# Optimization experiments

Hardware: AMD Instinct MI355X
Metric: run time of the kernel (lower is better)

The kernel has to match this reference:

```python
import jax, jax.numpy as jnp
import numpy as np

V, D, J = 1024, 1024, 1024  # num_outputs, predictor_dim, joiner_dim
B, U = 64, 512
NULL_INDEX = 0


def setup_inputs() -> dict:
    key = jax.random.key(0)
    ks = jax.random.split(key, 9)
    s = 0.02
    return {
        "y": jax.random.randint(ks[0], (B, U), 0, V, dtype=jnp.int64) if jax.config.jax_enable_x64 else jax.random.randint(ks[0], (B, U), 0, V, dtype=jnp.int32),
        "embed": jax.random.normal(ks[1], (V, D), jnp.float32) * s,
        "weight_ih": jax.random.normal(ks[2], (3 * D, D), jnp.float32) * s,
        "bias_ih": jax.random.normal(ks[3], (3 * D,), jnp.float32) * s,
        "weight_hh": jax.random.normal(ks[4], (3 * D, D), jnp.float32) * s,
        "bias_hh": jax.random.normal(ks[5], (3 * D,), jnp.float32) * s,
        "linear_w": jax.random.normal(ks[6], (J, D), jnp.float32) * s,
        "linear_b": jax.random.normal(ks[7], (J,), jnp.float32) * s,
        "initial_state": jax.random.normal(ks[8], (D,), jnp.float32),
    }


def reference(y, embed, weight_ih, bias_ih, weight_hh, bias_hh, linear_w, linear_b, initial_state):
    b, u_len = y.shape
    d = initial_state.shape[0]
    # Decoder input sequence: start symbol (NULL_INDEX=0) then the labels -> length U+1
    tokens = jnp.concatenate([jnp.full((b, 1), NULL_INDEX, dtype=y.dtype), y], axis=1)  # [B, U+1]
    x = embed[tokens]  # [B, U+1, D]
    # Precompute input-side gate pre-activations for all steps (batched GEMM)
    gx = jnp.einsum("bud,gd->bug", x, weight_ih) + bias_ih  # [B, U+1, 3D]
    h0 = jnp.broadcast_to(initial_state, (b, d))

    def step(h, gx_t):
        # PyTorch GRUCell: gates ordered (r, z, n)
        gh = h @ weight_hh.T + bias_hh  # [B, 3D]
        r = jax.nn.sigmoid(gx_t[:, :d] + gh[:, :d])
        z = jax.nn.sigmoid(gx_t[:, d:2 * d] + gh[:, d:2 * d])
        n = jnp.tanh(gx_t[:, 2 * d:] + r * gh[:, 2 * d:])
        h_new = (1.0 - z) * n + z * h
        return h_new, h_new

    _, hs = jax.lax.scan(step, h0, jnp.swapaxes(gx, 0, 1))  # hs: [U+1, B, D]
    out = jnp.einsum("ubd,jd->buj", hs, linear_w) + linear_b  # [B, U+1, J]
    return out
```

## Files before the change

### kernel.cpp

```cpp
#include <hip/hip_runtime.h>
#include <hip/hip_bf16.h>

typedef float f32x4 __attribute__((ext_vector_type(4)));
typedef short s16x8 __attribute__((ext_vector_type(8)));
typedef int   i32x4 __attribute__((ext_vector_type(4)));
typedef _Float16 h16x8 __attribute__((ext_vector_type(8)));

#define NV 1024
#define ND 1024
#define NJ 1024
#define NB 64
#define NU 512
#define NT 513
#define G3 3072
#define SLOT 65536
#define NWG 64
#define CANARY 0x7FFF7FFFu

static __device__ __forceinline__ unsigned short f2h(float f) {
  union { _Float16 h; unsigned short u; } x; x.h = (_Float16)f;
  return x.u;
}

static __device__ __forceinline__ void unswizzle(long e, int& r, int& k) {
  long blk = e >> 9; int l = (int)((e >> 3) & 63); int j = (int)(e & 7);
  r = (int)(blk >> 5) * 16 + (l & 15);
  k = ((int)(blk & 31)) * 32 + ((l >> 4) << 3) + j;
}

__global__ void predictor_prep(const float* __restrict__ whh, const float* __restrict__ wih,
                               const float* __restrict__ em, const float* __restrict__ lw,
                               const float* __restrict__ bih, const float* __restrict__ bhh,
                               const float* __restrict__ init,
                               unsigned short* __restrict__ wh_sw, unsigned short* __restrict__ wi_sw,
                               unsigned short* __restrict__ em_sw, unsigned short* __restrict__ lw_sw,
                               float* __restrict__ bias_sum, unsigned short* __restrict__ hs) {
  long e = (long)blockIdx.x * 256 + threadIdx.x;
  const long nbig = 3145728, nsm = 1048576;
  if (e < nbig) { int r, k; unswizzle(e, r, k); wh_sw[e] = f2h(whh[(long)r * 1024 + k]); return; }
  e -= nbig;
  if (e < nbig) { int r, k; unswizzle(e, r, k); wi_sw[e] = f2h(wih[(long)r * 1024 + k]); return; }
  e -= nbig;
  if (e < nsm) { int r, k; unswizzle(e, r, k); em_sw[e] = f2h(em[(long)r * 1024 + k]); return; }
  e -= nsm;
  if (e < nsm) { int r, k; unswizzle(e, r, k); lw_sw[e] = f2h(lw[(long)r * 1024 + k]); return; }
  e -= nsm;
  if (e < 65536) { int r, k; unswizzle(e, r, k); hs[e] = f2h(init[k]); return; }
  e -= 65536;
  if (e < 3072) { bias_sum[e] = bih[e] + bhh[e]; return; }
  e -= 3072;
  if (e < 4202496) {
    s16x8 c = { (short)0x7FFF, (short)0x7FFF, (short)0x7FFF, (short)0x7FFF,
                (short)0x7FFF, (short)0x7FFF, (short)0x7FFF, (short)0x7FFF };
    *(s16x8*)(hs + 65536 + e * 8) = c;
  }
}

__global__ __launch_bounds__(256) void predictor_gemm(
    const unsigned short* __restrict__ A, long a_chunk_stride,
    const unsigned short* __restrict__ Bw,
    const float* __restrict__ bias, float* __restrict__ out,
    int rowmul_i, int rowmul_c, int out_stride) {
  const int nt = blockIdx.x, chunk = blockIdx.y;
  const int tid = threadIdx.x, lane = tid & 63, wave = tid >> 6;
  const unsigned short* Ab = A + (long)chunk * a_chunk_stride + wave * 16384 + lane * 8;
  const unsigned short* Bb = Bw + (long)nt * 65536 + lane * 8;
  f32x4 a0 = {0,0,0,0}, a1 = {0,0,0,0}, a2 = {0,0,0,0}, a3 = {0,0,0,0};
#pragma unroll 4
  for (int kc = 0; kc < 32; ++kc) {
    h16x8 av = __builtin_bit_cast(h16x8, *(const s16x8*)(Ab + kc * 512));
    h16x8 w0 = __builtin_bit_cast(h16x8, *(const s16x8*)(Bb + kc * 512));
    h16x8 w1 = __builtin_bit_cast(h16x8, *(const s16x8*)(Bb + 16384 + kc * 512));
    h16x8 w2 = __builtin_bit_cast(h16x8, *(const s16x8*)(Bb + 32768 + kc * 512));
    h16x8 w3 = __builtin_bit_cast(h16x8, *(const s16x8*)(Bb + 49152 + kc * 512));
    a0 = __builtin_amdgcn_mfma_f32_16x16x32_f16(av, w0, a0, 0, 0, 0);
    a1 = __builtin_amdgcn_mfma_f32_16x16x32_f16(av, w1, a1, 0, 0, 0);
    a2 = __builtin_amdgcn_mfma_f32_16x16x32_f16(av, w2, a2, 0, 0, 0);
    a3 = __builtin_amdgcn_mfma_f32_16x16x32_f16(av, w3, a3, 0, 0, 0);
  }
  const int q = lane >> 4, nl = lane & 15, colbase = nt << 6;
#pragma unroll
  for (int j = 0; j < 4; ++j) {
    int il = (wave << 4) + (q << 2) + j;
    long row = (long)il * rowmul_i + (long)chunk * rowmul_c;
    float* orow = out + row * out_stride + colbase;
    orow[nl]      = a0[j] + bias[colbase + nl];
    orow[16 + nl] = a1[j] + bias[colbase + 16 + nl];
    orow[32 + nl] = a2[j] + bias[colbase + 32 + nl];
    orow[48 + nl] = a3[j] + bias[colbase + 48 + nl];
  }
}

#define PINSTAGE(CNT, B)                                                        \
  asm volatile("s_waitcnt vmcnt(" #CNT ")"                                      \
    : "+v"(hf[(B)*8+0]), "+v"(hf[(B)*8+1]), "+v"(hf[(B)*8+2]), "+v"(hf[(B)*8+3]), \
      "+v"(hf[(B)*8+4]), "+v"(hf[(B)*8+5]), "+v"(hf[(B)*8+6]), "+v"(hf[(B)*8+7]) :: "memory")

#define PVALID(B, CNT)                                                          \
  {                                                                             \
    PINSTAGE(CNT, B);                                                           \
    for (;;) {                                                                  \
      int ok = 1;                                                               \
      _Pragma("unroll")                                                         \
      for (int i = 0; i < 8; ++i) {                                             \
        i32x4 v = hf[(B)*8 + i];                                                \
        ok &= (v[0] != (int)CANARY) & (v[1] != (int)CANARY) &                   \
              (v[2] != (int)CANARY) & (v[3] != (int)CANARY);                    \
      }                                                                         \
      if (__all(ok)) break;                                                     \
      __builtin_amdgcn_s_sleep(1);                                              \
      _Pragma("unroll")                                                         \
      for (int i = 0; i < 8; ++i) {                                             \
        const unsigned short* a2_ = hprev + (B)*16384 + ((w<<3)+i)*512 + lane*8;\
        asm volatile("global_load_dwordx4 %0, %1, off sc1"                      \
                     : "=v"(hf[(B)*8+i]) : "v"(a2_) : "memory");                \
      }                                                                         \
      PINSTAGE(0, B);                                                           \
    }                                                                           \
  }

__global__ __launch_bounds__(256, 1) void predictor_rnn(
    const unsigned short* __restrict__ wh_sw, const float* __restrict__ gtab,
    const int* __restrict__ y, const float* __restrict__ init,
    unsigned short* __restrict__ hs) {
  __shared__ float buf[4][3][4][64][4];
  __shared__ unsigned short tbuf[1024];
  const int wg = blockIdx.x, tid = threadIdx.x, lane = tid & 63, w = tid >> 6;
  const int q = lane >> 4, dloc = lane & 15, dg = (wg << 4) + dloc;

  h16x8 wrf[8], wzf[8], wnf[8];
#pragma unroll
  for (int i = 0; i < 8; ++i) {
    int kc = (w << 3) + i;
    wrf[i] = __builtin_bit_cast(h16x8, *(const s16x8*)(wh_sw + ((long)(      wg) << 14) + kc * 512 + lane * 8));
    wzf[i] = __builtin_bit_cast(h16x8, *(const s16x8*)(wh_sw + ((long)( 64 + wg) << 14) + kc * 512 + lane * 8));
    wnf[i] = __builtin_bit_cast(h16x8, *(const s16x8*)(wh_sw + ((long)(128 + wg) << 14) + kc * 512 + lane * 8));
  }
  float hreg[4];
#pragma unroll
  for (int j = 0; j < 4; ++j) hreg[j] = init[dg];

  for (int t = 1; t <= NT; ++t) {
    float gr[4], gz[4], gn[4];
#pragma unroll
    for (int j = 0; j < 4; ++j) {
      int b = (w << 4) + (q << 2) + j;
      int tok = (t == 1) ? 0 : y[b * NU + (t - 2)];
      const float* g = gtab + (long)tok * G3 + dg;
      asm volatile("global_load_dword %0, %1, off" : "=v"(gr[j]) : "v"(g) : "memory");
      asm volatile("global_load_dword %0, %1, off" : "=v"(gz[j]) : "v"(g + 1024) : "memory");
      asm volatile("global_load_dword %0, %1, off" : "=v"(gn[j]) : "v"(g + 2048) : "memory");
    }

    const unsigned short* hprev = hs + (long)(t - 1) * SLOT;
    unsigned short* hcur = hs + (long)t * SLOT;

    i32x4 hf[32];
#pragma unroll
    for (int bg = 0; bg < 4; ++bg)
#pragma unroll
      for (int i = 0; i < 8; ++i) {
        const unsigned short* a = hprev + bg * 16384 + ((w << 3) + i) * 512 + lane * 8;
        asm volatile("global_load_dwordx4 %0, %1, off sc1" : "=v"(hf[bg * 8 + i]) : "v"(a) : "memory");
      }
    f32x4 aR[4], aZ[4], aN[4];
#pragma unroll
    for (int bg = 0; bg < 4; ++bg) { aR[bg] = (f32x4){0,0,0,0}; aZ[bg] = (f32x4){0,0,0,0}; aN[bg] = (f32x4){0,0,0,0}; }

    PVALID(0, 24);
#pragma unroll
    for (int i = 0; i < 8; ++i) { h16x8 a = __builtin_bit_cast(h16x8, hf[0 * 8 + i]);
      aR[0] = __builtin_amdgcn_mfma_f32_16x16x32_f16(a, wrf[i], aR[0], 0, 0, 0);
      aZ[0] = __builtin_amdgcn_mfma_f32_16x16x32_f16(a, wzf[i], aZ[0], 0, 0, 0);
      aN[0] = __builtin_amdgcn_mfma_f32_16x16x32_f16(a, wnf[i], aN[0], 0, 0, 0); }
    PVALID(1, 16);
#pragma unroll
    for (int i = 0; i < 8; ++i) { h16x8 a = __builtin_bit_cast(h16x8, hf[1 * 8 + i]);
      aR[1] = __builtin_amdgcn_mfma_f32_16x16x32_f16(a, wrf[i], aR[1], 0, 0, 0);
      aZ[1] = __builtin_amdgcn_mfma_f32_16x16x32_f16(a, wzf[i], aZ[1], 0, 0, 0);
      aN[1] = __builtin_amdgcn_mfma_f32_16x16x32_f16(a, wnf[i], aN[1], 0, 0, 0); }
    PVALID(2, 8);
#pragma unroll
    for (int i = 0; i < 8; ++i) { h16x8 a = __builtin_bit_cast(h16x8, hf[2 * 8 + i]);
      aR[2] = __builtin_amdgcn_mfma_f32_16x16x32_f16(a, wrf[i], aR[2], 0, 0, 0);
      aZ[2] = __builtin_amdgcn_mfma_f32_16x16x32_f16(a, wzf[i], aZ[2], 0, 0, 0);
      aN[2] = __builtin_amdgcn_mfma_f32_16x16x32_f16(a, wnf[i], aN[2], 0, 0, 0); }
    PVALID(3, 0);
#pragma unroll
    for (int i = 0; i < 8; ++i) { h16x8 a = __builtin_bit_cast(h16x8, hf[3 * 8 + i]);
      aR[3] = __builtin_amdgcn_mfma_f32_16x16x32_f16(a, wrf[i], aR[3], 0, 0, 0);
      aZ[3] = __builtin_amdgcn_mfma_f32_16x16x32_f16(a, wzf[i], aZ[3], 0, 0, 0);
      aN[3] = __builtin_amdgcn_mfma_f32_16x16x32_f16(a, wnf[i], aN[3], 0, 0, 0); }

    asm volatile("s_waitcnt vmcnt(0)"
      : "+v"(gr[0]), "+v"(gr[1]), "+v"(gr[2]), "+v"(gr[3]),
        "+v"(gz[0]), "+v"(gz[1]), "+v"(gz[2]), "+v"(gz[3]),
        "+v"(gn[0]), "+v"(gn[1]), "+v"(gn[2]), "+v"(gn[3]) :: "memory");

#pragma unroll
    for (int b2 = 0; b2 < 4; ++b2)
      if (b2 != w) {
        *(f32x4*)&buf[w][0][b2][lane][0] = aR[b2];
        *(f32x4*)&buf[w][1][b2][lane][0] = aZ[b2];
        *(f32x4*)&buf[w][2][b2][lane][0] = aN[b2];
      }
    __syncthreads();
    f32x4 sR = aR[w], sZ = aZ[w], sN = aN[w];
#pragma unroll
    for (int v = 0; v < 4; ++v)
      if (v != w) {
        sR += *(const f32x4*)&buf[v][0][w][lane][0];
        sZ += *(const f32x4*)&buf[v][1][w][lane][0];
        sN += *(const f32x4*)&buf[v][2][w][lane][0];
      }
    __syncthreads();

#pragma unroll
    for (int j = 0; j < 4; ++j) {
      float r = 1.f / (1.f + __expf(-(gr[j] + sR[j])));
      float z = 1.f / (1.f + __expf(-(gz[j] + sZ[j])));
      float np = gn[j] + r * sN[j];
      float e2 = __expf(-2.f * fabsf(np));
      float tn = (1.f - e2) / (1.f + e2);
      tn = np < 0.f ? -tn : tn;
      float hnew = (1.f - z) * tn + z * hreg[j];
      hreg[j] = hnew;
      tbuf[(w << 8) + ((((q << 2) + j) | ((dloc >> 3) << 4)) << 3) + (dloc & 7)] = f2h(hnew);
    }
    asm volatile("s_waitcnt lgkmcnt(0)" ::: "memory");

    {
      unsigned long long pv = *(const unsigned long long*)(tbuf + (w << 8) + lane * 4);
      unsigned short* gp = hcur + ((long)(w * 32 + (wg >> 1)) << 9) + ((wg & 1) << 8) + lane * 4;
      asm volatile("global_store_dwordx2 %0, %1, off sc1" :: "v"(gp), "v"(pv) : "memory");
    }
  }
}

extern "C" void kernel_launch(void* const* d_in, const int* in_sizes, int n_in,
                              void* d_out, int out_size, void* d_ws, size_t ws_size,
                              hipStream_t stream) {
  const int*   y    = (const int*)d_in[0];
  const float* em   = (const float*)d_in[1];
  const float* wih  = (const float*)d_in[2];
  const float* bih  = (const float*)d_in[3];
  const float* whh  = (const float*)d_in[4];
  const float* bhh  = (const float*)d_in[5];
  const float* lw   = (const float*)d_in[6];
  const float* lb   = (const float*)d_in[7];
  const float* init = (const float*)d_in[8];
  float* out = (float*)d_out;

  char* ws = (char*)d_ws;
  size_t off = 0;
  auto alloc = [&](size_t n) { void* p = ws + off; off += (n + 255) & ~(size_t)255; return p; };
  unsigned short* wh_sw   = (unsigned short*)alloc(6291456);
  unsigned short* wi_sw   = (unsigned short*)alloc(6291456);
  unsigned short* em_sw   = (unsigned short*)alloc(2097152);
  unsigned short* lw_sw   = (unsigned short*)alloc(2097152);
  float*          gtab    = (float*)alloc(12582912);
  float*          bias_sum= (float*)alloc(12288);
  unsigned short* hs      = (unsigned short*)alloc(67371008UL);
  (void)ws_size; (void)in_sizes; (void)n_in; (void)out_size;

  predictor_prep<<<dim3(49452), dim3(256), 0, stream>>>(
      whh, wih, em, lw, bih, bhh, init, wh_sw, wi_sw, em_sw, lw_sw, bias_sum, hs);
  predictor_gemm<<<dim3(48, 16), dim3(256), 0, stream>>>(
      em_sw, 65536L, wi_sw, bias_sum, gtab, 1, 64, 3072);
  predictor_rnn<<<dim3(NWG), dim3(256), 0, stream>>>(wh_sw, gtab, y, init, hs);
  predictor_gemm<<<dim3(16, 513), dim3(256), 0, stream>>>(
      hs + 65536, 65536L, lw_sw, lb, out, 513, 1, 1024);
}
```

Before: 3.425 ms.

## Fuse output projection into RNN kernel with per-step flag-driven consumer workgroups

Merges the recurrent GRU kernel and the final output-projection GEMM into one persistent launch. 64 workgroups run the recurrence and publish a per-wave step counter in padded flag slots, and 192 extra workgroups poll those flags and compute output tiles for finished timesteps while later steps are still running. The RNN workgroups now also wait on the flags of all producer waves before loading the previous hidden state, in addition to the existing canary check. This hides the output GEMM behind the serial recurrence, at the cost of polling traffic, more memory contention on the RNN critical path, and a dependence on all 256 workgroups being co-resident.

```diff
diff --git a/kernel.cpp b/kernel.cpp
--- a/kernel.cpp
+++ b/kernel.cpp
@@ -15,6 +15,9 @@
 #define G3 3072
 #define SLOT 65536
 #define NWG 64
+#define NOUT 192
+#define NTILE 8208
+#define FSTRIDE 32
 #define CANARY 0x7FFF7FFFu
 
 static __device__ __forceinline__ unsigned short f2h(float f) {
@@ -34,7 +37,8 @@
                                const float* __restrict__ init,
                                unsigned short* __restrict__ wh_sw, unsigned short* __restrict__ wi_sw,
                                unsigned short* __restrict__ em_sw, unsigned short* __restrict__ lw_sw,
-                               float* __restrict__ bias_sum, unsigned short* __restrict__ hs) {
+                               float* __restrict__ bias_sum, unsigned short* __restrict__ hs,
+                               unsigned int* __restrict__ flags) {
   long e = (long)blockIdx.x * 256 + threadIdx.x;
   const long nbig = 3145728, nsm = 1048576;
   if (e < nbig) { int r, k; unswizzle(e, r, k); wh_sw[e] = f2h(whh[(long)r * 1024 + k]); return; }
@@ -49,7 +53,9 @@
   e -= 65536;
   if (e < 3072) { bias_sum[e] = bih[e] + bhh[e]; return; }
   e -= 3072;
-  if (e < 4202496) {
+  if (e < 8192) { flags[e] = 0u; return; }
+  e -= 8192;
+  if (e < 4202752) {
     s16x8 c = { (short)0x7FFF, (short)0x7FFF, (short)0x7FFF, (short)0x7FFF,
                 (short)0x7FFF, (short)0x7FFF, (short)0x7FFF, (short)0x7FFF };
     *(s16x8*)(hs + 65536 + e * 8) = c;
@@ -119,120 +125,205 @@
     }                                                                           \
   }
 
-__global__ __launch_bounds__(256, 1) void predictor_rnn(
+__global__ __launch_bounds__(256, 1) void predictor_fused(
     const unsigned short* __restrict__ wh_sw, const float* __restrict__ gtab,
     const int* __restrict__ y, const float* __restrict__ init,
-    unsigned short* __restrict__ hs) {
+    unsigned short* __restrict__ hs, unsigned int* __restrict__ flags,
+    const unsigned short* __restrict__ lw_sw, const float* __restrict__ lb,
+    float* __restrict__ out) {
   __shared__ float buf[4][3][4][64][4];
   __shared__ unsigned short tbuf[1024];
   const int wg = blockIdx.x, tid = threadIdx.x, lane = tid & 63, w = tid >> 6;
-  const int q = lane >> 4, dloc = lane & 15, dg = (wg << 4) + dloc;
-
-  h16x8 wrf[8], wzf[8], wnf[8];
-#pragma unroll
-  for (int i = 0; i < 8; ++i) {
-    int kc = (w << 3) + i;
-    wrf[i] = __builtin_bit_cast(h16x8, *(const s16x8*)(wh_sw + ((long)(      wg) << 14) + kc * 512 + lane * 8));
-    wzf[i] = __builtin_bit_cast(h16x8, *(const s16x8*)(wh_sw + ((long)( 64 + wg) << 14) + kc * 512 + lane * 8));
-    wnf[i] = __builtin_bit_cast(h16x8, *(const s16x8*)(wh_sw + ((long)(128 + wg) << 14) + kc * 512 + lane * 8));
-  }
-  float hreg[4];
-#pragma unroll
-  for (int j = 0; j < 4; ++j) hreg[j] = init[dg];
-
-  for (int t = 1; t <= NT; ++t) {
-    float gr[4], gz[4], gn[4];
+
+  if (wg < NWG) {
+    const int q = lane >> 4, dloc = lane & 15, dg = (wg << 4) + dloc;
+
+    h16x8 wrf[8], wzf[8], wnf[8];
+#pragma unroll
+    for (int i = 0; i < 8; ++i) {
+      int kc = (w << 3) + i;
+      wrf[i] = __builtin_bit_cast(h16x8, *(const s16x8*)(wh_sw + ((long)(      wg) << 14) + kc * 512 + lane * 8));
+      wzf[i] = __builtin_bit_cast(h16x8, *(const s16x8*)(wh_sw + ((long)( 64 + wg) << 14) + kc * 512 + lane * 8));
+      wnf[i] = __builtin_bit_cast(h16x8, *(const s16x8*)(wh_sw + ((long)(128 + wg) << 14) + kc * 512 + lane * 8));
+    }
+    float hreg[4];
+#pragma unroll
+    for (int j = 0; j < 4; ++j) hreg[j] = init[dg];
+
+    for (int t = 1; t <= NT; ++t) {
+      float gr[4], gz[4], gn[4];
+#pragma unroll
+      for (int j = 0; j < 4; ++j) {
+        int b = (w << 4) + (q << 2) + j;
+        int tok = (t == 1) ? 0 : y[b * NU + (t - 2)];
+        const float* g = gtab + (long)tok * G3 + dg;
+        asm volatile("global_load_dword %0, %1, off" : "=v"(gr[j]) : "v"(g) : "memory");
+        asm volatile("global_load_dword %0, %1, off" : "=v"(gz[j]) : "v"(g + 1024) : "memory");
+        asm volatile("global_load_dword %0, %1, off" : "=v"(gn[j]) : "v"(g + 2048) : "memory");
+      }
+
+      if (t > 1) {
+        const unsigned int* fp = flags + (unsigned)((w << 6) + lane) * FSTRIDE;
+        const unsigned int tm1 = (unsigned)(t - 1);
+        for (;;) {
+          unsigned int v;
+          asm volatile("global_load_dword %0, %1, off sc1" : "=v"(v) : "v"(fp) : "memory");
+          asm volatile("s_waitcnt vmcnt(0)" : "+v"(v) :: "memory");
+          if (__all((int)(v >= tm1))) break;
+          __builtin_amdgcn_s_sleep(1);
+        }
+      }
+      asm volatile("s_waitcnt vmcnt(0)"
+        : "+v"(gr[0]), "+v"(gr[1]), "+v"(gr[2]), "+v"(gr[3]),
+          "+v"(gz[0]), "+v"(gz[1]), "+v"(gz[2]), "+v"(gz[3]),
+          "+v"(gn[0]), "+v"(gn[1]), "+v"(gn[2]), "+v"(gn[3]) :: "memory");
+
+      const unsigned short* hprev = hs + (long)(t - 1) * SLOT;
+      unsigned short* hcur = hs + (long)t * SLOT;
+
+      i32x4 hf[32];
+#pragma unroll
+      for (int bg = 0; bg < 4; ++bg)
+#pragma unroll
+        for (int i = 0; i < 8; ++i) {
+          const unsigned short* a = hprev + bg * 16384 + ((w << 3) + i) * 512 + lane * 8;
+          asm volatile("global_load_dwordx4 %0, %1, off sc1" : "=v"(hf[bg * 8 + i]) : "v"(a) : "memory");
+        }
+      f32x4 aR[4], aZ[4], aN[4];
+#pragma unroll
+      for (int bg = 0; bg < 4; ++bg) { aR[bg] = (f32x4){0,0,0,0}; aZ[bg] = (f32x4){0,0,0,0}; aN[bg] = (f32x4){0,0,0,0}; }
+
+      PVALID(0, 24);
+#pragma unroll
+      for (int i = 0; i < 8; ++i) { h16x8 a = __builtin_bit_cast(h16x8, hf[0 * 8 + i]);
+        aR[0] = __builtin_amdgcn_mfma_f32_16x16x32_f16(a, wrf[i], aR[0], 0, 0, 0);
+        aZ[0] = __builtin_amdgcn_mfma_f32_16x16x32_f16(a, wzf[i], aZ[0], 0, 0, 0);
+        aN[0] = __builtin_amdgcn_mfma_f32_16x16x32_f16(a, wnf[i], aN[0], 0, 0, 0); }
+      PVALID(1, 16);
+#pragma unroll
+      for (int i = 0; i < 8; ++i) { h16x8 a = __builtin_bit_cast(h16x8, hf[1 * 8 + i]);
+        aR[1] = __builtin_amdgcn_mfma_f32_16x16x32_f16(a, wrf[i], aR[1], 0, 0, 0);
+        aZ[1] = __builtin_amdgcn_mfma_f32_16x16x32_f16(a, wzf[i], aZ[1], 0, 0, 0);
+        aN[1] = __builtin_amdgcn_mfma_f32_16x16x32_f16(a, wnf[i], aN[1], 0, 0, 0); }
+      PVALID(2, 8);
+#pragma unroll
+      for (int i = 0; i < 8; ++i) { h16x8 a = __builtin_bit_cast(h16x8, hf[2 * 8 + i]);
+        aR[2] = __builtin_amdgcn_mfma_f32_16x16x32_f16(a, wrf[i], aR[2], 0, 0, 0);
+        aZ[2] = __builtin_amdgcn_mfma_f32_16x16x32_f16(a, wzf[i], aZ[2], 0, 0, 0);
+        aN[2] = __builtin_amdgcn_mfma_f32_16x16x32_f16(a, wnf[i], aN[2], 0, 0, 0); }
+      PVALID(3, 0);
+#pragma unroll
+      for (int i = 0; i < 8; ++i) { h16x8 a = __builtin_bit_cast(h16x8, hf[3 * 8 + i]);
+        aR[3] = __builtin_amdgcn_mfma_f32_16x16x32_f16(a, wrf[i], aR[3], 0, 0, 0);
+        aZ[3] = __builtin_amdgcn_mfma_f32_16x16x32_f16(a, wzf[i], aZ[3], 0, 0, 0);
+        aN[3] = __builtin_amdgcn_mfma_f32_16x16x32_f16(a, wnf[i], aN[3], 0, 0, 0); }
+
+#pragma unroll
+      for (int b2 = 0; b2 < 4; ++b2)
+        if (b2 != w) {
+          *(f32x4*)&buf[w][0][b2][lane][0] = aR[b2];
+          *(f32x4*)&buf[w][1][b2][lane][0] = aZ[b2];
+          *(f32x4*)&buf[w][2][b2][lane][0] = aN[b2];
+        }
+      __syncthreads();
+      f32x4 sR = aR[w], sZ = aZ[w], sN = aN[w];
+#pragma unroll
+      for (int v = 0; v < 4; ++v)
+        if (v != w) {
+          sR += *(const f32x4*)&buf[v][0][w][lane][0];
+          sZ += *(const f32x4*)&buf[v][1][w][lane][0];
+          sN += *(const f32x4*)&buf[v][2][w][lane][0];
+        }
+      __syncthreads();
+
+#pragma unroll
+      for (int j = 0; j < 4; ++j) {
+        float r = 1.f / (1.f + __expf(-(gr[j] + sR[j])));
+        float z = 1.f / (1.f + __expf(-(gz[j] + sZ[j])));
+        float np = gn[j] + r * sN[j];
+        float e2 = __expf(-2.f * fabsf(np));
+        float tn = (1.f - e2) / (1.f + e2);
+        tn = np < 0.f ? -tn : tn;
+        float hnew = (1.f - z) * tn + z * hreg[j];
+        hreg[j] = hnew;
+        tbuf[(w << 8) + ((((q << 2) + j) | ((dloc >> 3) << 4)) << 3) + (dloc & 7)] = f2h(hnew);
+      }
+      asm volatile("s_waitcnt lgkmcnt(0)" ::: "memory");
+
+      {
+        unsigned long long pv = *(const unsigned long long*)(tbuf + (w << 8) + lane * 4);
+        unsigned short* gp = hcur + ((long)(w * 32 + (wg >> 1)) << 9) + ((wg & 1) << 8) + lane * 4;
+        asm volatile("global_store_dwordx2 %0, %1, off sc1" :: "v"(gp), "v"(pv) : "memory");
+        if (lane == 0)
+          __hip_atomic_store(&flags[((wg << 2) + w) * FSTRIDE], (unsigned)t,
+                             __ATOMIC_RELAXED, __HIP_MEMORY_SCOPE_AGENT);
+      }
+    }
+    return;
+  }
+
+  const int g = wg - NWG;
+  for (int k = g; k < NTILE; k += NOUT) {
+    const int t = k >> 4, nt = k & 15;
+    const unsigned st = (unsigned)(t + 1);
+
+    if (w == 0) {
+      const unsigned int* fp = flags + lane * 4 * FSTRIDE;
+      for (;;) {
+        unsigned v0, v1, v2, v3;
+        asm volatile("global_load_dword %0, %1, off sc1" : "=v"(v0) : "v"(fp + 0 * FSTRIDE) : "memory");
+        asm volatile("global_load_dword %0, %1, off sc1" : "=v"(v1) : "v"(fp + 1 * FSTRIDE) : "memory");
+        asm volatile("global_load_dword %0, %1, off sc1" : "=v"(v2) : "v"(fp + 2 * FSTRIDE) : "memory");
+        asm volatile("global_load_dword %0, %1, off sc1" : "=v"(v3) : "v"(fp + 3 * FSTRIDE) : "memory");
+        asm volatile("s_waitcnt vmcnt(0)" : "+v"(v0), "+v"(v1), "+v"(v2), "+v"(v3) :: "memory");
+        if (__all((int)((v0 >= st) & (v1 >= st) & (v2 >= st) & (v3 >= st)))) break;
+        __builtin_amdgcn_s_sleep(64);
+      }
+    }
+    __syncthreads();
+
+    const unsigned short* Ab = hs + (long)st * SLOT + w * 16384 + lane * 8;
+    i32x4 hf[32];
+    for (;;) {
+#pragma unroll
+      for (int kc = 0; kc < 32; ++kc)
+        asm volatile("global_load_dwordx4 %0, %1, off sc1" : "=v"(hf[kc]) : "v"(Ab + kc * 512) : "memory");
+      PINSTAGE(0, 0); PINSTAGE(0, 1); PINSTAGE(0, 2); PINSTAGE(0, 3);
+      int ok = 1;
+#pragma unroll
+      for (int kc = 0; kc < 32; ++kc) {
+        i32x4 v = hf[kc];
+        ok &= (v[0] != (int)CANARY) & (v[1] != (int)CANARY) &
+              (v[2] != (int)CANARY) & (v[3] != (int)CANARY);
+      }
+      if (__all(ok)) break;
+      __builtin_amdgcn_s_sleep(8);
+    }
+
+    const unsigned short* Bb = lw_sw + (long)nt * 65536 + lane * 8;
+    f32x4 a0 = {0,0,0,0}, a1 = {0,0,0,0}, a2 = {0,0,0,0}, a3 = {0,0,0,0};
+#pragma unroll 4
+    for (int kc = 0; kc < 32; ++kc) {
+      h16x8 av = __builtin_bit_cast(h16x8, hf[kc]);
+      h16x8 w0 = __builtin_bit_cast(h16x8, *(const s16x8*)(Bb + kc * 512));
+      h16x8 w1 = __builtin_bit_cast(h16x8, *(const s16x8*)(Bb + 16384 + kc * 512));
+      h16x8 w2 = __builtin_bit_cast(h16x8, *(const s16x8*)(Bb + 32768 + kc * 512));
+      h16x8 w3 = __builtin_bit_cast(h16x8, *(const s16x8*)(Bb + 49152 + kc * 512));
+      a0 = __builtin_amdgcn_mfma_f32_16x16x32_f16(av, w0, a0, 0, 0, 0);
+      a1 = __builtin_amdgcn_mfma_f32_16x16x32_f16(av, w1, a1, 0, 0, 0);
+      a2 = __builtin_amdgcn_mfma_f32_16x16x32_f16(av, w2, a2, 0, 0, 0);
+      a3 = __builtin_amdgcn_mfma_f32_16x16x32_f16(av, w3, a3, 0, 0, 0);
+    }
+    const int qq = lane >> 4, nl = lane & 15, colbase = nt << 6;
 #pragma unroll
     for (int j = 0; j < 4; ++j) {
-      int b = (w << 4) + (q << 2) + j;
-      int tok = (t == 1) ? 0 : y[b * NU + (t - 2)];
-      const float* g = gtab + (long)tok * G3 + dg;
-      asm volatile("global_load_dword %0, %1, off" : "=v"(gr[j]) : "v"(g) : "memory");
-      asm volatile("global_load_dword %0, %1, off" : "=v"(gz[j]) : "v"(g + 1024) : "memory");
-      asm volatile("global_load_dword %0, %1, off" : "=v"(gn[j]) : "v"(g + 2048) : "memory");
-    }
-
-    const unsigned short* hprev = hs + (long)(t - 1) * SLOT;
-    unsigned short* hcur = hs + (long)t * SLOT;
-
-    i32x4 hf[32];
-#pragma unroll
-    for (int bg = 0; bg < 4; ++bg)
-#pragma unroll
-      for (int i = 0; i < 8; ++i) {
-        const unsigned short* a = hprev + bg * 16384 + ((w << 3) + i) * 512 + lane * 8;
-        asm volatile("global_load_dwordx4 %0, %1, off sc1" : "=v"(hf[bg * 8 + i]) : "v"(a) : "memory");
-      }
-    f32x4 aR[4], aZ[4], aN[4];
-#pragma unroll
-    for (int bg = 0; bg < 4; ++bg) { aR[bg] = (f32x4){0,0,0,0}; aZ[bg] = (f32x4){0,0,0,0}; aN[bg] = (f32x4){0,0,0,0}; }
-
-    PVALID(0, 24);
-#pragma unroll
-    for (int i = 0; i < 8; ++i) { h16x8 a = __builtin_bit_cast(h16x8, hf[0 * 8 + i]);
-      aR[0] = __builtin_amdgcn_mfma_f32_16x16x32_f16(a, wrf[i], aR[0], 0, 0, 0);
-      aZ[0] = __builtin_amdgcn_mfma_f32_16x16x32_f16(a, wzf[i], aZ[0], 0, 0, 0);
-      aN[0] = __builtin_amdgcn_mfma_f32_16x16x32_f16(a, wnf[i], aN[0], 0, 0, 0); }
-    PVALID(1, 16);
-#pragma unroll
-    for (int i = 0; i < 8; ++i) { h16x8 a = __builtin_bit_cast(h16x8, hf[1 * 8 + i]);
-      aR[1] = __builtin_amdgcn_mfma_f32_16x16x32_f16(a, wrf[i], aR[1], 0, 0, 0);
-      aZ[1] = __builtin_amdgcn_mfma_f32_16x16x32_f16(a, wzf[i], aZ[1], 0, 0, 0);
-      aN[1] = __builtin_amdgcn_mfma_f32_16x16x32_f16(a, wnf[i], aN[1], 0, 0, 0); }
-    PVALID(2, 8);
-#pragma unroll
-    for (int i = 0; i < 8; ++i) { h16x8 a = __builtin_bit_cast(h16x8, hf[2 * 8 + i]);
-      aR[2] = __builtin_amdgcn_mfma_f32_16x16x32_f16(a, wrf[i], aR[2], 0, 0, 0);
-      aZ[2] = __builtin_amdgcn_mfma_f32_16x16x32_f16(a, wzf[i], aZ[2], 0, 0, 0);
-      aN[2] = __builtin_amdgcn_mfma_f32_16x16x32_f16(a, wnf[i], aN[2], 0, 0, 0); }
-    PVALID(3, 0);
-#pragma unroll
-    for (int i = 0; i < 8; ++i) { h16x8 a = __builtin_bit_cast(h16x8, hf[3 * 8 + i]);
-      aR[3] = __builtin_amdgcn_mfma_f32_16x16x32_f16(a, wrf[i], aR[3], 0, 0, 0);
-      aZ[3] = __builtin_amdgcn_mfma_f32_16x16x32_f16(a, wzf[i], aZ[3], 0, 0, 0);
-      aN[3] = __builtin_amdgcn_mfma_f32_16x16x32_f16(a, wnf[i], aN[3], 0, 0, 0); }
-
-    asm volatile("s_waitcnt vmcnt(0)"
-      : "+v"(gr[0]), "+v"(gr[1]), "+v"(gr[2]), "+v"(gr[3]),
-        "+v"(gz[0]), "+v"(gz[1]), "+v"(gz[2]), "+v"(gz[3]),
-        "+v"(gn[0]), "+v"(gn[1]), "+v"(gn[2]), "+v"(gn[3]) :: "memory");
-
-#pragma unroll
-    for (int b2 = 0; b2 < 4; ++b2)
-      if (b2 != w) {
-        *(f32x4*)&buf[w][0][b2][lane][0] = aR[b2];
-        *(f32x4*)&buf[w][1][b2][lane][0] = aZ[b2];
-        *(f32x4*)&buf[w][2][b2][lane][0] = aN[b2];
-      }
-    __syncthreads();
-    f32x4 sR = aR[w], sZ = aZ[w], sN = aN[w];
-#pragma unroll
-    for (int v = 0; v < 4; ++v)
-      if (v != w) {
-        sR += *(const f32x4*)&buf[v][0][w][lane][0];
-        sZ += *(const f32x4*)&buf[v][1][w][lane][0];
-        sN += *(const f32x4*)&buf[v][2][w][lane][0];
-      }
-    __syncthreads();
-
-#pragma unroll
-    for (int j = 0; j < 4; ++j) {
-      float r = 1.f / (1.f + __expf(-(gr[j] + sR[j])));
-      float z = 1.f / (1.f + __expf(-(gz[j] + sZ[j])));
-      float np = gn[j] + r * sN[j];
-      float e2 = __expf(-2.f * fabsf(np));
-      float tn = (1.f - e2) / (1.f + e2);
-      tn = np < 0.f ? -tn : tn;
-      float hnew = (1.f - z) * tn + z * hreg[j];
-      hreg[j] = hnew;
-      tbuf[(w << 8) + ((((q << 2) + j) | ((dloc >> 3) << 4)) << 3) + (dloc & 7)] = f2h(hnew);
-    }
-    asm volatile("s_waitcnt lgkmcnt(0)" ::: "memory");
-
-    {
-      unsigned long long pv = *(const unsigned long long*)(tbuf + (w << 8) + lane * 4);
-      unsigned short* gp = hcur + ((long)(w * 32 + (wg >> 1)) << 9) + ((wg & 1) << 8) + lane * 4;
-      asm volatile("global_store_dwordx2 %0, %1, off sc1" :: "v"(gp), "v"(pv) : "memory");
+      int il = (w << 4) + (qq << 2) + j;
+      long row = (long)il * 513 + t;
+      float* orow = out + row * 1024 + colbase;
+      orow[nl]      = a0[j] + lb[colbase + nl];
+      orow[16 + nl] = a1[j] + lb[colbase + 16 + nl];
+      orow[32 + nl] = a2[j] + lb[colbase + 32 + nl];
+      orow[48 + nl] = a3[j] + lb[colbase + 48 + nl];
     }
   }
 }
@@ -260,14 +351,14 @@
   unsigned short* lw_sw   = (unsigned short*)alloc(2097152);
   float*          gtab    = (float*)alloc(12582912);
   float*          bias_sum= (float*)alloc(12288);
+  unsigned int*   flags   = (unsigned int*)alloc(32768);
   unsigned short* hs      = (unsigned short*)alloc(67371008UL);
   (void)ws_size; (void)in_sizes; (void)n_in; (void)out_size;
 
-  predictor_prep<<<dim3(49452), dim3(256), 0, stream>>>(
-      whh, wih, em, lw, bih, bhh, init, wh_sw, wi_sw, em_sw, lw_sw, bias_sum, hs);
+  predictor_prep<<<dim3(49485), dim3(256), 0, stream>>>(
+      whh, wih, em, lw, bih, bhh, init, wh_sw, wi_sw, em_sw, lw_sw, bias_sum, hs, flags);
   predictor_gemm<<<dim3(48, 16), dim3(256), 0, stream>>>(
       em_sw, 65536L, wi_sw, bias_sum, gtab, 1, 64, 3072);
-  predictor_rnn<<<dim3(NWG), dim3(256), 0, stream>>>(wh_sw, gtab, y, init, hs);
-  predictor_gemm<<<dim3(16, 513), dim3(256), 0, stream>>>(
-      hs + 65536, 65536L, lw_sw, lb, out, 513, 1, 1024);
-}
+  predictor_fused<<<dim3(NWG + NOUT), dim3(256), 0, stream>>>(
+      wh_sw, gtab, y, init, hs, flags, lw_sw, lb, out);
+}
```

New measurement: 3.626 ms. 1.06x slower.
